# Kernel tuning notes

Hardware: AMD Instinct MI355X
Metric: run time of the kernel (lower is better)

## Reference

```python
import jax, jax.numpy as jnp
import numpy as np
from jax.ops import segment_sum, segment_max

N_NODES = 50000
N_EDGES = 800000
D_IN = 128
HEADS = 4
D_HEAD = 32
OUT_DIM = 512
NEG_SLOPE = 0.2
EPS = 1e-9


def setup_inputs() -> dict:
    key = jax.random.key(0)
    ks = jax.random.split(key, 12)
    h = jax.random.normal(ks[0], (N_NODES, D_IN), dtype=jnp.float32)
    src = jax.random.randint(ks[1], (N_EDGES,), 0, N_NODES, dtype=jnp.int32)
    dst = jax.random.randint(ks[2], (N_EDGES,), 0, N_NODES, dtype=jnp.int32)
    s = 0.1
    W1 = jax.random.normal(ks[3], (D_IN, HEADS * D_HEAD), dtype=jnp.float32) * s
    al1 = jax.random.normal(ks[4], (HEADS, D_HEAD), dtype=jnp.float32) * s
    ar1 = jax.random.normal(ks[5], (HEADS, D_HEAD), dtype=jnp.float32) * s
    b1 = jnp.zeros((HEADS * D_HEAD,), dtype=jnp.float32)
    W2 = jax.random.normal(ks[6], (HEADS * D_HEAD, HEADS * D_HEAD), dtype=jnp.float32) * s
    al2 = jax.random.normal(ks[7], (HEADS, D_HEAD), dtype=jnp.float32) * s
    ar2 = jax.random.normal(ks[8], (HEADS, D_HEAD), dtype=jnp.float32) * s
    b2 = jnp.zeros((HEADS * D_HEAD,), dtype=jnp.float32)
    Wp = jax.random.normal(ks[9], (D_HEAD, OUT_DIM), dtype=jnp.float32) * s
    bp = jnp.zeros((OUT_DIM,), dtype=jnp.float32)
    return {"h": h, "src": src, "dst": dst, "W1": W1, "al1": al1, "ar1": ar1,
            "b1": b1, "W2": W2, "al2": al2, "ar2": ar2, "b2": b2,
            "Wp": Wp, "bp": bp}


def gat_layer(h, W, a_l, a_r, b, src, dst, agg):
    # h: [N, Din]; W: [Din, H*Dh]; a_l/a_r: [H, Dh]; b: [H*Dh]
    N = h.shape[0]
    Wh = (h @ W).reshape(N, HEADS, D_HEAD)            # [N, H, Dh]
    el = jnp.einsum('nhd,hd->nh', Wh, a_l)            # [N, H]
    er = jnp.einsum('nhd,hd->nh', Wh, a_r)            # [N, H]
    e = el[src] + er[dst]                             # [E, H]
    e = jnp.where(e > 0, e, NEG_SLOPE * e)            # LeakyReLU(0.2)
    m = segment_max(e, dst, num_segments=N)           # [N, H]
    m = jnp.where(jnp.isfinite(m), m, 0.0)            # empty segments
    ex = jnp.exp(e - m[dst])                          # [E, H]
    denom = segment_sum(ex, dst, num_segments=N)      # [N, H]
    alpha = ex / (denom[dst] + EPS)                   # [E, H]
    msg = alpha[:, :, None] * Wh[src]                 # [E, H, Dh]
    out = segment_sum(msg, dst, num_segments=N)       # [N, H, Dh]
    out = out + b.reshape(HEADS, D_HEAD)
    if agg == 'flatten':
        return out.reshape(N, HEADS * D_HEAD)
    return out.mean(axis=1)                           # 'mean' for last layer


def reference(h, src, dst, W1, al1, ar1, b1, W2, al2, ar2, b2, Wp, bp):
    src = src.astype(jnp.int32)
    dst = dst.astype(jnp.int32)
    z = gat_layer(h, W1, al1, ar1, b1, src, dst, agg='flatten')
    z = jax.nn.elu(z)
    z = gat_layer(z, W2, al2, ar2, b2, src, dst, agg='mean')  # [N, Dh]
    return z @ Wp + bp                                        # [N, OUT_DIM]
```

## Files before the change

### kernel.cpp

```cpp
#include <hip/hip_runtime.h>
#include <hip/hip_bf16.h>
#include <math.h>

#define HEADS 4
#define D_HEAD 32
#define HD 128
#define D_IN 128
#define OUT_DIM 512
#define NEG_SLOPE 0.2f
#define EPS 1e-9f
#define LOG2E 1.4426950408889634f
#define MAXD 64

typedef float f32x4 __attribute__((ext_vector_type(4)));
typedef float f32x2 __attribute__((ext_vector_type(2)));
typedef short bf16x8 __attribute__((ext_vector_type(8)));
typedef unsigned short u16x8 __attribute__((ext_vector_type(8)));

#if defined(__has_builtin)
#if __has_builtin(__builtin_amdgcn_exp2f)
#define EXP2(x) __builtin_amdgcn_exp2f(x)
#else
#define EXP2(x) exp2f(x)
#endif
#else
#define EXP2(x) exp2f(x)
#endif

__device__ __forceinline__ float lrelu(float x) { return x > 0.f ? x : NEG_SLOPE * x; }

__device__ __forceinline__ unsigned short f2bf(float f)
{
    union { float f; unsigned int u; } v; v.f = f;
    unsigned int r = (v.u + 0x7FFFu + ((v.u >> 16) & 1u)) >> 16;
    return (unsigned short)r;
}
__device__ __forceinline__ float bf2f(unsigned short b)
{
    union { unsigned int u; float f; } v; v.u = ((unsigned int)b) << 16;
    return v.f;
}

__global__ void setup(const float* __restrict__ W1, const float* __restrict__ W2,
                      unsigned short* __restrict__ Wt1, unsigned short* __restrict__ Wt2,
                      int* __restrict__ cnt, int N)
{
    int idx = blockIdx.x * 256 + threadIdx.x;
    if (idx < 16384) {
        int k = idx >> 7, c = idx & 127;
        Wt1[(size_t)c * 128 + k] = f2bf(W1[idx]);
    } else if (idx < 32768) {
        int i = idx - 16384;
        int k = i >> 7, c = i & 127;
        Wt2[(size_t)c * 128 + k] = f2bf(W2[i]);
    } else {
        int i = idx - 32768;
        if (i < N) cnt[i] = 0;
    }
}

template <int BF16IN>
__device__ __forceinline__ void gemm_core(
    unsigned short* Xs, unsigned short* Wts, int tid, int node0,
    const void* __restrict__ Xv, const unsigned short* __restrict__ Wt,
    const float* __restrict__ al, const float* __restrict__ ar,
    unsigned short* __restrict__ Wh, float* __restrict__ el, float* __restrict__ er, int N)
{
    {
        const uint4* src = (const uint4*)Wt;
#pragma unroll
        for (int i = 0; i < 8; ++i) {
            int f = tid + 256 * i;
            int row = f >> 4;
            int byte = (f << 4) ^ ((row & 7) << 4);
            *(uint4*)((char*)Wts + byte) = src[f];
        }
    }
    {
#pragma unroll
        for (int i = 0; i < 2; ++i) {
            int f = tid + 256 * i;
            int row = f >> 4, kc = f & 15;
            int n = node0 + row;
            int byte = (f << 4) ^ ((row & 7) << 4);
            if (BF16IN) {
                uint4 v = make_uint4(0, 0, 0, 0);
                if (n < N)
                    v = *(const uint4*)((const unsigned short*)Xv + (size_t)n * 128 + kc * 8);
                *(uint4*)((char*)Xs + byte) = v;
            } else {
                u16x8 v = {0, 0, 0, 0, 0, 0, 0, 0};
                if (n < N) {
                    const float* xp = (const float*)Xv + (size_t)n * 128 + kc * 8;
                    float4 f0 = *(const float4*)xp;
                    float4 f1 = *(const float4*)(xp + 4);
                    v[0] = f2bf(f0.x); v[1] = f2bf(f0.y); v[2] = f2bf(f0.z); v[3] = f2bf(f0.w);
                    v[4] = f2bf(f1.x); v[5] = f2bf(f1.y); v[6] = f2bf(f1.z); v[7] = f2bf(f1.w);
                }
                *(u16x8*)((char*)Xs + byte) = v;
            }
        }
    }
    __syncthreads();

    const int w  = tid >> 6;
    const int l  = tid & 63;
    const int lr = l & 15;
    const int lg = l >> 4;

    f32x4 zero4 = {0.f, 0.f, 0.f, 0.f};
    f32x4 acc[2][2];
    acc[0][0] = zero4; acc[0][1] = zero4; acc[1][0] = zero4; acc[1][1] = zero4;

    const int c0 = w * 32 + lr, c1 = w * 32 + 16 + lr;
    const int rA0 = lr, rA1 = 16 + lr;

#pragma unroll
    for (int ks = 0; ks < 4; ++ks) {
        const int kb2 = ks * 64 + lg * 16;
        bf16x8 a0 = *(const bf16x8*)((char*)Xs  + ((rA0 * 256 + kb2) ^ ((rA0 & 7) << 4)));
        bf16x8 a1 = *(const bf16x8*)((char*)Xs  + ((rA1 * 256 + kb2) ^ ((rA1 & 7) << 4)));
        bf16x8 b0 = *(const bf16x8*)((char*)Wts + ((c0  * 256 + kb2) ^ ((c0  & 7) << 4)));
        bf16x8 b1 = *(const bf16x8*)((char*)Wts + ((c1  * 256 + kb2) ^ ((c1  & 7) << 4)));
        acc[0][0] = __builtin_amdgcn_mfma_f32_16x16x32_bf16(a0, b0, acc[0][0], 0, 0, 0);
        acc[0][1] = __builtin_amdgcn_mfma_f32_16x16x32_bf16(a0, b1, acc[0][1], 0, 0, 0);
        acc[1][0] = __builtin_amdgcn_mfma_f32_16x16x32_bf16(a1, b0, acc[1][0], 0, 0, 0);
        acc[1][1] = __builtin_amdgcn_mfma_f32_16x16x32_bf16(a1, b1, acc[1][1], 0, 0, 0);
    }

    const float alv0 = al[w * 32 + lr], alv1 = al[w * 32 + 16 + lr];
    const float arv0 = ar[w * 32 + lr], arv1 = ar[w * 32 + 16 + lr];

#pragma unroll
    for (int rt = 0; rt < 2; ++rt) {
#pragma unroll
        for (int r = 0; r < 4; ++r) {
            const int n = node0 + rt * 16 + lg * 4 + r;
            if (n < N) {
                Wh[(size_t)n * 128 + w * 32 + lr]      = f2bf(acc[rt][0][r]);
                Wh[(size_t)n * 128 + w * 32 + 16 + lr] = f2bf(acc[rt][1][r]);
            }
            float pl = acc[rt][0][r] * alv0 + acc[rt][1][r] * alv1;
            float pr = acc[rt][0][r] * arv0 + acc[rt][1][r] * arv1;
#pragma unroll
            for (int off = 1; off < 16; off <<= 1) {
                pl += __shfl_xor(pl, off, 16);
                pr += __shfl_xor(pr, off, 16);
            }
            if (lr == 0 && n < N) {
                el[(size_t)n * 4 + w] = pl;
                er[(size_t)n * 4 + w] = pr;
            }
        }
    }
}

__global__ __launch_bounds__(256) void gemm1_scatter(
    const float* __restrict__ h, const unsigned short* __restrict__ Wt1,
    const float* __restrict__ al, const float* __restrict__ ar,
    unsigned short* __restrict__ Wh, float* __restrict__ el, float* __restrict__ er, int N,
    const int* __restrict__ src, const int* __restrict__ dst,
    int* __restrict__ cnt, int* __restrict__ colp, int E, int GB)
{
    __shared__ unsigned short Xs[32 * 128];
    __shared__ unsigned short Wts[128 * 128];

    if (blockIdx.x < GB) {
        gemm_core<0>(Xs, Wts, threadIdx.x, blockIdx.x * 32, h, Wt1, al, ar, Wh, el, er, N);
        return;
    }
    int t = (blockIdx.x - GB) * 256 + threadIdx.x;
    int base = t * 4;
    if (base >= E) return;
    if (base + 4 <= E) {
        int4 s4 = ((const int4*)src)[t];
        int4 d4 = ((const int4*)dst)[t];
        int p;
        p = atomicAdd(&cnt[d4.x], 1); if (p < MAXD) colp[(size_t)d4.x * MAXD + p] = s4.x;
        p = atomicAdd(&cnt[d4.y], 1); if (p < MAXD) colp[(size_t)d4.y * MAXD + p] = s4.y;
        p = atomicAdd(&cnt[d4.z], 1); if (p < MAXD) colp[(size_t)d4.z * MAXD + p] = s4.z;
        p = atomicAdd(&cnt[d4.w], 1); if (p < MAXD) colp[(size_t)d4.w * MAXD + p] = s4.w;
    } else {
        for (int e = base; e < E; ++e) {
            int d = dst[e];
            int p = atomicAdd(&cnt[d], 1);
            if (p < MAXD) colp[(size_t)d * MAXD + p] = src[e];
        }
    }
}

__global__ __launch_bounds__(256) void gemm_mfma2(
    const unsigned short* __restrict__ z, const unsigned short* __restrict__ Wt2,
    const float* __restrict__ al, const float* __restrict__ ar,
    unsigned short* __restrict__ Wh, float* __restrict__ el, float* __restrict__ er, int N)
{
    __shared__ unsigned short Xs[32 * 128];
    __shared__ unsigned short Wts[128 * 128];
    gemm_core<1>(Xs, Wts, threadIdx.x, blockIdx.x * 32, z, Wt2, al, ar, Wh, el, er, N);
}

template <int MODE>
__global__ __launch_bounds__(256) void gat_node(
    const int* __restrict__ cnt, const int* __restrict__ colp,
    const float* __restrict__ el, const float* __restrict__ er,
    const unsigned short* __restrict__ Wh, const float* __restrict__ bias,
    void* __restrict__ out, int N)
{
    const int wave = threadIdx.x >> 6;
    const int lane = threadIdx.x & 63;
    const int n = blockIdx.x * 4 + wave;
    if (n >= N) return;

    const int deg   = min(cnt[n], MAXD);
    const int start = n * MAXD;
    const int end   = start + deg;

    const int g  = lane >> 4;
    const int r  = lane & 15;
    const int h2 = r >> 2;
    const float erv = er[(size_t)n * 4 + h2];

    float accA[8] = {0.f, 0.f, 0.f, 0.f, 0.f, 0.f, 0.f, 0.f};
    float accB[8] = {0.f, 0.f, 0.f, 0.f, 0.f, 0.f, 0.f, 0.f};
    float dA = 0.f, dB = 0.f;

#define GAT_EDGE(JJ, ACC, DEN) do {                                            \
        int s_ = colp[(JJ)];                                                   \
        float e_ = lrelu(el[(size_t)s_ * 4 + h2] + erv);                       \
        float p_ = EXP2(e_ * LOG2E);                                           \
        u16x8 w_ = *(const u16x8*)(Wh + (size_t)s_ * 128 + 8 * r);             \
        ACC[0] += p_ * bf2f(w_[0]); ACC[1] += p_ * bf2f(w_[1]);                \
        ACC[2] += p_ * bf2f(w_[2]); ACC[3] += p_ * bf2f(w_[3]);                \
        ACC[4] += p_ * bf2f(w_[4]); ACC[5] += p_ * bf2f(w_[5]);                \
        ACC[6] += p_ * bf2f(w_[6]); ACC[7] += p_ * bf2f(w_[7]);                \
        DEN += p_;                                                             \
    } while (0)

    int j = start + g;
    for (; j + 4 < end; j += 8) {
        GAT_EDGE(j, accA, dA);
        GAT_EDGE(j + 4, accB, dB);
    }
    if (j < end) GAT_EDGE(j, accA, dA);
#undef GAT_EDGE

    float acc[8];
#pragma unroll
    for (int i = 0; i < 8; ++i) acc[i] = accA[i] + accB[i];
    float den = dA + dB;

#pragma unroll
    for (int i = 0; i < 8; ++i) {
        acc[i] += __shfl_xor(acc[i], 16, 64);
        acc[i] += __shfl_xor(acc[i], 32, 64);
    }
    den += __shfl_xor(den, 16, 64);
    den += __shfl_xor(den, 32, 64);

    const float inv = 1.f / (den + EPS);
    const float4 bv0 = *(const float4*)(bias + 8 * r);
    const float4 bv1 = *(const float4*)(bias + 8 * r + 4);
    float x[8];
    x[0] = acc[0] * inv + bv0.x; x[1] = acc[1] * inv + bv0.y;
    x[2] = acc[2] * inv + bv0.z; x[3] = acc[3] * inv + bv0.w;
    x[4] = acc[4] * inv + bv1.x; x[5] = acc[5] * inv + bv1.y;
    x[6] = acc[6] * inv + bv1.z; x[7] = acc[7] * inv + bv1.w;

    if (MODE == 0) {
        if (g == 0) {
            u16x8 ob;
#pragma unroll
            for (int i = 0; i < 8; ++i) {
                float v = x[i] > 0.f ? x[i] : expm1f(x[i]);
                ob[i] = f2bf(v);
            }
            *(u16x8*)((unsigned short*)out + (size_t)n * 128 + 8 * r) = ob;
        }
    } else {
#pragma unroll
        for (int i = 0; i < 8; ++i) {
            x[i] += __shfl_xor(x[i], 4, 64);
            x[i] += __shfl_xor(x[i], 8, 64);
        }
        if (g == 0 && r < 4) {
            float4 o0 = make_float4(0.25f * x[0], 0.25f * x[1], 0.25f * x[2], 0.25f * x[3]);
            float4 o1 = make_float4(0.25f * x[4], 0.25f * x[5], 0.25f * x[6], 0.25f * x[7]);
            *(float4*)((float*)out + (size_t)n * 32 + 8 * r)     = o0;
            *(float4*)((float*)out + (size_t)n * 32 + 8 * r + 4) = o1;
        }
    }
}

#define PROJ_NB 2048
__device__ __forceinline__ void proj_load(const float* __restrict__ z2, int n, float4* z)
{
#pragma unroll
    for (int i = 0; i < 8; ++i)
        z[i] = *(const float4*)(z2 + (size_t)n * 32 + i * 4);
}

__device__ __forceinline__ f32x2 proj_comp(const float4* z, const float2* wp, float2 bv)
{
    float x = bv.x, y = bv.y;
#pragma unroll
    for (int k4 = 0; k4 < 8; ++k4) {
        float4 zz = z[k4];
        x += zz.x * wp[4 * k4 + 0].x; y += zz.x * wp[4 * k4 + 0].y;
        x += zz.y * wp[4 * k4 + 1].x; y += zz.y * wp[4 * k4 + 1].y;
        x += zz.z * wp[4 * k4 + 2].x; y += zz.z * wp[4 * k4 + 2].y;
        x += zz.w * wp[4 * k4 + 3].x; y += zz.w * wp[4 * k4 + 3].y;
    }
    f32x2 o; o.x = x; o.y = y;
    return o;
}

__global__ __launch_bounds__(256) void proj(
    const float* __restrict__ z2, const float* __restrict__ Wp,
    const float* __restrict__ bp, float* __restrict__ out, int N)
{
    const int wave = threadIdx.x >> 6;
    const int lane = threadIdx.x & 63;
    const int c0 = wave * 128 + lane * 2;

    const int per = (N + PROJ_NB - 1) / PROJ_NB;
    int n  = blockIdx.x * per;
    const int nE = min(n + per, N);
    if (n >= nE) return;

    float2 wp[32];
#pragma unroll
    for (int k = 0; k < 32; ++k)
        wp[k] = *(const float2*)(Wp + (size_t)k * 512 + c0);
    const float2 bv = *(const float2*)(bp + c0);

    float4 zA[8], zB[8];
    proj_load(z2, n, zA);

    for (; n + 2 <= nE; n += 2) {
        proj_load(z2, n + 1, zB);
        f32x2 oA = proj_comp(zA, wp, bv);
        __builtin_nontemporal_store(oA, (f32x2*)(out + (size_t)n * 512 + c0));
        if (n + 2 < nE) proj_load(z2, n + 2, zA);
        f32x2 oB = proj_comp(zB, wp, bv);
        __builtin_nontemporal_store(oB, (f32x2*)(out + (size_t)(n + 1) * 512 + c0));
    }
    if (n < nE) {
        f32x2 oA = proj_comp(zA, wp, bv);
        __builtin_nontemporal_store(oA, (f32x2*)(out + (size_t)n * 512 + c0));
    }
}

extern "C" void kernel_launch(void* const* d_in, const int* in_sizes, int n_in,
                              void* d_out, int out_size, void* d_ws, size_t ws_size,
                              hipStream_t stream)
{
    const float* h   = (const float*)d_in[0];
    const int*   src = (const int*)d_in[1];
    const int*   dst = (const int*)d_in[2];
    const float* W1  = (const float*)d_in[3];
    const float* al1 = (const float*)d_in[4];
    const float* ar1 = (const float*)d_in[5];
    const float* b1  = (const float*)d_in[6];
    const float* W2  = (const float*)d_in[7];
    const float* al2 = (const float*)d_in[8];
    const float* ar2 = (const float*)d_in[9];
    const float* b2  = (const float*)d_in[10];
    const float* Wp  = (const float*)d_in[11];
    const float* bp  = (const float*)d_in[12];
    float* out = (float*)d_out;

    const int N = in_sizes[0] / D_IN;
    const int E = in_sizes[1];

    float* ws = (float*)d_ws;
    size_t off = 0;
    unsigned short* Wh = (unsigned short*)(ws + off); off += (size_t)N * 64;
    unsigned short* z  = (unsigned short*)(ws + off); off += (size_t)N * 64;
    float* z2   = ws + off; off += (size_t)N * 32;
    float* el   = ws + off; off += (size_t)N * 4;
    float* er   = ws + off; off += (size_t)N * 4;
    int* cnt    = (int*)(ws + off); off += (size_t)N;
    int* colp   = (int*)(ws + off); off += (size_t)N * MAXD;
    unsigned short* Wt1 = (unsigned short*)(ws + off); off += 8192;
    unsigned short* Wt2 = (unsigned short*)(ws + off); off += 8192;

    const int gemm_grid = (N + 31) / 32;
    const int scat_grid = ((E + 3) / 4 + 255) / 256;
    const int node_grid = (N + 3) / 4;

    setup<<<(32768 + N + 255) / 256, 256, 0, stream>>>(W1, W2, Wt1, Wt2, cnt, N);

    gemm1_scatter<<<gemm_grid + scat_grid, 256, 0, stream>>>(
        h, Wt1, al1, ar1, Wh, el, er, N, src, dst, cnt, colp, E, gemm_grid);

    gat_node<0><<<node_grid, 256, 0, stream>>>(cnt, colp, el, er, Wh, b1, z, N);

    gemm_mfma2<<<gemm_grid, 256, 0, stream>>>(z, Wt2, al2, ar2, Wh, el, er, N);
    gat_node<1><<<node_grid, 256, 0, stream>>>(cnt, colp, el, er, Wh, b2, z2, N);

    proj<<<PROJ_NB, 256, 0, stream>>>(z2, Wp, bp, out, N);
}
```

Measured before the change: 306.5 us.

## Store adjacency as 16-bit indices and split scatter from first GEMM

Column indices in the padded adjacency are now stored as unsigned short instead of int, halving adjacency storage and the bytes read per edge in both aggregation kernels. The edge scatter moves out of the fused gemm1 launch into its own kernel, one edge per thread, and both GEMMs share a templated kernel. This adds a separate launch and drops the overlap between scatter and the first GEMM. The 16-bit indices only hold node ids up to 65535, so it relies on N staying under that bound.

Measured after the change: 307.3 us. About the same (+0.3%).

```diff
diff --git a/kernel.cpp b/kernel.cpp
--- a/kernel.cpp
+++ b/kernel.cpp
@@ -57,6 +57,16 @@
         int i = idx - 32768;
         if (i < N) cnt[i] = 0;
     }
+}
+
+__global__ void scatter_padded(const int* __restrict__ src, const int* __restrict__ dst,
+                               int* __restrict__ cnt, unsigned short* __restrict__ colp, int E)
+{
+    int e = blockIdx.x * 256 + threadIdx.x;
+    if (e >= E) return;
+    int d = dst[e];
+    int p = atomicAdd(&cnt[d], 1);
+    if (p < MAXD) colp[(size_t)d * MAXD + p] = (unsigned short)src[e];
 }
 
 template <int BF16IN>
@@ -155,53 +165,20 @@
     }
 }
 
-__global__ __launch_bounds__(256) void gemm1_scatter(
-    const float* __restrict__ h, const unsigned short* __restrict__ Wt1,
+template <int BF16IN>
+__global__ __launch_bounds__(256) void gemm_mfma(
+    const void* __restrict__ Xv, const unsigned short* __restrict__ Wt,
     const float* __restrict__ al, const float* __restrict__ ar,
-    unsigned short* __restrict__ Wh, float* __restrict__ el, float* __restrict__ er, int N,
-    const int* __restrict__ src, const int* __restrict__ dst,
-    int* __restrict__ cnt, int* __restrict__ colp, int E, int GB)
+    unsigned short* __restrict__ Wh, float* __restrict__ el, float* __restrict__ er, int N)
 {
     __shared__ unsigned short Xs[32 * 128];
     __shared__ unsigned short Wts[128 * 128];
-
-    if (blockIdx.x < GB) {
-        gemm_core<0>(Xs, Wts, threadIdx.x, blockIdx.x * 32, h, Wt1, al, ar, Wh, el, er, N);
-        return;
-    }
-    int t = (blockIdx.x - GB) * 256 + threadIdx.x;
-    int base = t * 4;
-    if (base >= E) return;
-    if (base + 4 <= E) {
-        int4 s4 = ((const int4*)src)[t];
-        int4 d4 = ((const int4*)dst)[t];
-        int p;
-        p = atomicAdd(&cnt[d4.x], 1); if (p < MAXD) colp[(size_t)d4.x * MAXD + p] = s4.x;
-        p = atomicAdd(&cnt[d4.y], 1); if (p < MAXD) colp[(size_t)d4.y * MAXD + p] = s4.y;
-        p = atomicAdd(&cnt[d4.z], 1); if (p < MAXD) colp[(size_t)d4.z * MAXD + p] = s4.z;
-        p = atomicAdd(&cnt[d4.w], 1); if (p < MAXD) colp[(size_t)d4.w * MAXD + p] = s4.w;
-    } else {
-        for (int e = base; e < E; ++e) {
-            int d = dst[e];
-            int p = atomicAdd(&cnt[d], 1);
-            if (p < MAXD) colp[(size_t)d * MAXD + p] = src[e];
-        }
-    }
-}
-
-__global__ __launch_bounds__(256) void gemm_mfma2(
-    const unsigned short* __restrict__ z, const unsigned short* __restrict__ Wt2,
-    const float* __restrict__ al, const float* __restrict__ ar,
-    unsigned short* __restrict__ Wh, float* __restrict__ el, float* __restrict__ er, int N)
-{
-    __shared__ unsigned short Xs[32 * 128];
-    __shared__ unsigned short Wts[128 * 128];
-    gemm_core<1>(Xs, Wts, threadIdx.x, blockIdx.x * 32, z, Wt2, al, ar, Wh, el, er, N);
+    gemm_core<BF16IN>(Xs, Wts, threadIdx.x, blockIdx.x * 32, Xv, Wt, al, ar, Wh, el, er, N);
 }
 
 template <int MODE>
 __global__ __launch_bounds__(256) void gat_node(
-    const int* __restrict__ cnt, const int* __restrict__ colp,
+    const int* __restrict__ cnt, const unsigned short* __restrict__ colp,
     const float* __restrict__ el, const float* __restrict__ er,
     const unsigned short* __restrict__ Wh, const float* __restrict__ bias,
     void* __restrict__ out, int N)
@@ -225,7 +202,7 @@
     float dA = 0.f, dB = 0.f;
 
 #define GAT_EDGE(JJ, ACC, DEN) do {                                            \
-        int s_ = colp[(JJ)];                                                   \
+        int s_ = (int)colp[(JJ)];                                              \
         float e_ = lrelu(el[(size_t)s_ * 4 + h2] + erv);                       \
         float p_ = EXP2(e_ * LOG2E);                                           \
         u16x8 w_ = *(const u16x8*)(Wh + (size_t)s_ * 128 + 8 * r);             \
@@ -380,22 +357,21 @@
     float* el   = ws + off; off += (size_t)N * 4;
     float* er   = ws + off; off += (size_t)N * 4;
     int* cnt    = (int*)(ws + off); off += (size_t)N;
-    int* colp   = (int*)(ws + off); off += (size_t)N * MAXD;
+    unsigned short* colp = (unsigned short*)(ws + off); off += (size_t)N * MAXD / 2;
     unsigned short* Wt1 = (unsigned short*)(ws + off); off += 8192;
     unsigned short* Wt2 = (unsigned short*)(ws + off); off += 8192;
 
     const int gemm_grid = (N + 31) / 32;
-    const int scat_grid = ((E + 3) / 4 + 255) / 256;
+    const int edge_grid = (E + 255) / 256;
     const int node_grid = (N + 3) / 4;
 
     setup<<<(32768 + N + 255) / 256, 256, 0, stream>>>(W1, W2, Wt1, Wt2, cnt, N);
-
-    gemm1_scatter<<<gemm_grid + scat_grid, 256, 0, stream>>>(
-        h, Wt1, al1, ar1, Wh, el, er, N, src, dst, cnt, colp, E, gemm_grid);
-
+    scatter_padded<<<edge_grid, 256, 0, stream>>>(src, dst, cnt, colp, E);
+
+    gemm_mfma<0><<<gemm_grid, 256, 0, stream>>>(h, Wt1, al1, ar1, Wh, el, er, N);
     gat_node<0><<<node_grid, 256, 0, stream>>>(cnt, colp, el, er, Wh, b1, z, N);
 
-    gemm_mfma2<<<gemm_grid, 256, 0, stream>>>(z, Wt2, al2, ar2, Wh, el, er, N);
+    gemm_mfma<1><<<gemm_grid, 256, 0, stream>>>(z, Wt2, al2, ar2, Wh, el, er, N);
     gat_node<1><<<node_grid, 256, 0, stream>>>(cnt, colp, el, er, Wh, b2, z2, N);
 
     proj<<<PROJ_NB, 256, 0, stream>>>(z2, Wp, bp, out, N);
```
